# Optimization experiments

Measured on AMD Instinct MI355X. Metric: run time of the kernel, lower is better.

## Reference

```python
import jax, jax.numpy as jnp
import numpy as np

NUM_HEADS = 4
NEG_INF = -1e9  # finite large-negative to avoid inf*weight -> nan in head combiner


def setup_inputs() -> dict:
    key = jax.random.key(0)
    k1, k2, k3, k4, k5 = jax.random.split(key, 5)
    B, S, T = 16, 1024, 512
    Q, E = 256, 512
    src_encodings = jax.random.normal(k1, (B, S, E), dtype=jnp.float32)
    src_token_mask = jax.random.randint(k2, (B, S), 0, 2).astype(jnp.bool_)
    query_vec = jax.random.normal(k3, (T, B, Q), dtype=jnp.float32)
    # Linear(src_encoding_size, query_vec_size * numheads, bias=False)
    W_src = jax.random.normal(k4, (E, Q * NUM_HEADS), dtype=jnp.float32) * (1.0 / np.sqrt(E))
    # Linear(numheads, 1, bias=False) -> combiner vector of shape (numheads,)
    w_comb = jax.random.normal(k5, (NUM_HEADS,), dtype=jnp.float32) * 0.5
    return {"src_encodings": src_encodings, "src_token_mask": src_token_mask,
            "query_vec": query_vec, "W_src": W_src, "w_comb": w_comb}


def reference(src_encodings, src_token_mask, query_vec, W_src, w_comb):
    # project + leaky_relu: (B,S,E) @ (E,H*Q) -> (B,S,H*Q)
    proj = jax.nn.leaky_relu(src_encodings @ W_src)
    B, S, _ = proj.shape
    Q = query_vec.shape[-1]
    proj = proj.reshape(B, S, NUM_HEADS, Q)                 # (B,S,H,Q)
    # per-head attention scores against each query step: (T,B,S,H)
    scores = jnp.einsum('bshq,tbq->tbsh', proj, query_vec)
    # mask invalid source tokens along S (broadcast over T and heads)
    scores = jnp.where(src_token_mask[None, :, :, None], NEG_INF, scores)
    # multihead combiner Linear(H,1,bias=False): (T,B,S)
    weights = jnp.einsum('tbsh,h->tbs', scores, w_comb)
    return jax.nn.softmax(weights, axis=-1)
```

## Files before the change

### kernel.cpp

```cpp
#include <hip/hip_runtime.h>
#include <hip/hip_bf16.h>
#include <cstdint>

constexpr int Bn = 16;
constexpr int Sn = 1024;
constexpr int Tn = 512;
constexpr int QD = 256;
constexpr int En = 512;
constexpr int Hn = 4;
constexpr float SLOPE = 0.01f;
constexpr float NEG_INF = -1e9f;
constexpr int Mn = Bn * Sn;

typedef _Float16 f16;
typedef f16 f16x4 __attribute__((ext_vector_type(4)));
typedef f16 f16x8 __attribute__((ext_vector_type(8)));
typedef float f32x4 __attribute__((ext_vector_type(4)));

#define G2L(g, l) __builtin_amdgcn_global_load_lds(                      \
    (const __attribute__((address_space(1))) void*)(g),                  \
    (__attribute__((address_space(3))) void*)(l), 16, 0, 0)

#define VM4 asm volatile("s_waitcnt vmcnt(4)" ::: "memory")
#define VM0 asm volatile("s_waitcnt vmcnt(0)" ::: "memory")

__global__ void detect_mask_kernel(const unsigned char* __restrict__ mask_bytes,
                                   int* __restrict__ flag) {
    __shared__ int cnt;
    if (threadIdx.x == 0) cnt = 0;
    __syncthreads();
    int local = 0;
    for (int p = threadIdx.x; p < 4096; p += 256) {
        if ((p & 3) != 0 && mask_bytes[p] != 0) local++;
    }
    atomicAdd(&cnt, local);
    __syncthreads();
    if (threadIdx.x == 0) flag[0] = (cnt == 0) ? 1 : 0;
}

__global__ __launch_bounds__(256) void conv_a_kernel(
    const float* __restrict__ src, f16* __restrict__ Ah, f16* __restrict__ Al)
{
    const size_t i4 = (size_t)blockIdx.x * 256 + threadIdx.x;
    const size_t base = i4 * 4;
    const float4 v = *(const float4*)(src + base);
    f16x4 hi, lo;
    const float xs[4] = {v.x, v.y, v.z, v.w};
    #pragma unroll
    for (int j = 0; j < 4; ++j) {
        f16 h = (f16)xs[j];
        hi[j] = h;
        lo[j] = (f16)(xs[j] - (float)h);
    }
    *(f16x4*)(Ah + base) = hi;
    *(f16x4*)(Al + base) = lo;
}

__global__ __launch_bounds__(256) void conv_b_kernel(
    const float* __restrict__ W, f16* __restrict__ Bht, f16* __restrict__ Blt)
{
    __shared__ float T[64][65];
    const int tid = threadIdx.x;
    const int n0 = blockIdx.x * 64;
    const int k0 = blockIdx.y * 64;
    #pragma unroll
    for (int p = 0; p < 4; ++p) {
        const int e = p * 256 + tid;
        const int r = e >> 4;
        const int c4 = e & 15;
        const float4 v = *(const float4*)(W + (size_t)(k0 + r) * (Hn * QD) + n0 + c4 * 4);
        T[r][c4 * 4 + 0] = v.x; T[r][c4 * 4 + 1] = v.y;
        T[r][c4 * 4 + 2] = v.z; T[r][c4 * 4 + 3] = v.w;
    }
    __syncthreads();
    #pragma unroll
    for (int p = 0; p < 4; ++p) {
        const int e = p * 256 + tid;
        const int r = e >> 4;
        const int c4 = e & 15;
        f16x4 hi, lo;
        #pragma unroll
        for (int j = 0; j < 4; ++j) {
            const float x = T[c4 * 4 + j][r];
            f16 h = (f16)x;
            hi[j] = h;
            lo[j] = (f16)(x - (float)h);
        }
        const size_t off = (size_t)(n0 + r) * En + k0 + c4 * 4;
        *(f16x4*)(Bht + off) = hi;
        *(f16x4*)(Blt + off) = lo;
    }
}

__global__ __launch_bounds__(256) void conv_q_kernel(
    const float* __restrict__ query, f16* __restrict__ Qh, f16* __restrict__ Ql)
{
    const int tid = threadIdx.x;
    const int rloc = tid >> 6;
    const int lane = tid & 63;
    const int row = blockIdx.x * 4 + rloc;
    const int t = row >> 4, b = row & 15;
    const float4 v = *(const float4*)(query + (size_t)row * QD + lane * 4);
    f16x4 hi, lo;
    const float xs[4] = {v.x, v.y, v.z, v.w};
    #pragma unroll
    for (int j = 0; j < 4; ++j) {
        f16 h = (f16)xs[j];
        hi[j] = h;
        lo[j] = (f16)(xs[j] - (float)h);
    }
    const size_t off = ((size_t)(b * Tn + t)) * QD + lane * 4;
    *(f16x4*)(Qh + off) = hi;
    *(f16x4*)(Ql + off) = lo;
}

__global__ __launch_bounds__(256) void gemm1_kernel(
    const f16* __restrict__ Ah, const f16* __restrict__ Al,
    const f16* __restrict__ Bht, const f16* __restrict__ Blt,
    const float* __restrict__ wcomb,
    f16* __restrict__ Ch, f16* __restrict__ Cl)
{
    __shared__ f16 lds_f[24576];

    const int tid = threadIdx.x;
    const int l  = tid & 63;
    const int wv = tid >> 6;
    const int wm = wv >> 1;
    const int wn = wv & 1;
    const int m0 = blockIdx.x * 128;
    const int q0 = blockIdx.y * 32;

    const int rowc = tid >> 2;
    const int xk   = ((tid & 3) ^ ((rowc >> 1) & 3)) * 8;
    const int stgA = (m0 + rowc) * En + xk;
    const int nB   = ((rowc >> 4) & 3) * QD + q0 + (rowc & 15);
    const int stgB = nB * En + xk;

    const int xf  = ((l >> 1) & 3);
    const int aFrag = (wm * 64 + (l & 15)) * 32 + (((l >> 4) ^ xf) * 8);
    const int bFrag = 4096 + (wn * 64 + (l & 15)) * 32 + (((l >> 4) ^ xf) * 8);

    f32x4 acc[4][4];
    #pragma unroll
    for (int m = 0; m < 4; ++m)
        #pragma unroll
        for (int h = 0; h < 4; ++h) acc[m][h] = (f32x4){0.f, 0.f, 0.f, 0.f};

    auto stage1 = [&](int t) {
        const f16* As = (t < 16) ? Ah : ((t < 32) ? Al : Ah);
        const f16* Bs = (t < 32) ? Bht : Blt;
        const int kofs = (t & 15) * 32;
        f16* dst = lds_f + (t % 3) * 8192 + wv * 512;
        G2L(As + stgA + kofs,           dst);
        G2L(As + stgA + 64 * En + kofs, dst + 2048);
        G2L(Bs + stgB + kofs,           dst + 4096);
        G2L(Bs + stgB + 16 * En + kofs, dst + 4096 + 2048);
    };

    stage1(0);
    stage1(1);
    VM4;
    __builtin_amdgcn_s_barrier();

    #pragma unroll
    for (int t = 0; t < 48; ++t) {
        const f16* Lb = lds_f + (t % 3) * 8192;
        f16x8 af[4], bfr[4];
        #pragma unroll
        for (int m = 0; m < 4; ++m) af[m] = *(const f16x8*)(Lb + aFrag + m * 512);
        #pragma unroll
        for (int h = 0; h < 4; ++h) bfr[h] = *(const f16x8*)(Lb + bFrag + h * 512);
        if (t + 2 < 48) stage1(t + 2);
        __builtin_amdgcn_s_barrier();
        asm volatile("s_waitcnt lgkmcnt(0)" ::: "memory");
        __builtin_amdgcn_sched_barrier(0);
        __builtin_amdgcn_s_setprio(1);
        #pragma unroll
        for (int m = 0; m < 4; ++m) {
            #pragma unroll
            for (int h = 0; h < 4; ++h)
                acc[m][h] = __builtin_amdgcn_mfma_f32_16x16x32_f16(
                    af[m], bfr[h], acc[m][h], 0, 0, 0);
        }
        __builtin_amdgcn_s_setprio(0);
        if (t <= 45)      VM4;
        else if (t == 46) VM0;
        __builtin_amdgcn_s_barrier();
    }

    const float w0 = wcomb[0], w1 = wcomb[1], w2 = wcomb[2], w3 = wcomb[3];
    const int q = q0 + wn * 16 + (l & 15);
    const int rbase = m0 + wm * 64 + (l >> 4) * 4;
    #pragma unroll
    for (int m = 0; m < 4; ++m) {
        #pragma unroll
        for (int i = 0; i < 4; ++i) {
            float x0 = acc[m][0][i]; x0 = x0 >= 0.f ? x0 : SLOPE * x0;
            float x1 = acc[m][1][i]; x1 = x1 >= 0.f ? x1 : SLOPE * x1;
            float x2 = acc[m][2][i]; x2 = x2 >= 0.f ? x2 : SLOPE * x2;
            float x3 = acc[m][3][i]; x3 = x3 >= 0.f ? x3 : SLOPE * x3;
            const float c = w0 * x0 + w1 * x1 + w2 * x2 + w3 * x3;
            const f16 ch = (f16)c;
            const f16 cl = (f16)(c - (float)ch);
            const size_t off = (size_t)(rbase + m * 16 + i) * QD + q;
            Ch[off] = ch;
            Cl[off] = cl;
        }
    }
}

__global__ __launch_bounds__(256) void gemm2_kernel(
    const f16* __restrict__ Ch, const f16* __restrict__ Cl,
    const f16* __restrict__ Qh, const f16* __restrict__ Ql,
    const void* __restrict__ maskp, const float* __restrict__ wcomb,
    const int* __restrict__ flag,
    float* __restrict__ out)
{
    __shared__ f16 lds2[24576];

    const int tid = threadIdx.x;
    const int l  = tid & 63;
    const int wv = tid >> 6;
    const int wm = wv >> 1;
    const int wn = wv & 1;
    const int b  = blockIdx.z;
    const int s0 = blockIdx.x * 128;
    const int t0 = blockIdx.y * 128;

    const int rowc = tid >> 2;
    const int xk   = ((tid & 3) ^ ((rowc >> 1) & 3)) * 8;
    const int stgA = (b * Sn + s0 + rowc) * QD + xk;
    const int stgB = (b * Tn + t0 + rowc) * QD + xk;

    const int xf  = ((l >> 1) & 3);
    const int aFrag = (wm * 64 + (l & 15)) * 32 + (((l >> 4) ^ xf) * 8);
    const int bFrag = 4096 + (wn * 64 + (l & 15)) * 32 + (((l >> 4) ^ xf) * 8);

    f32x4 acc[4][4];
    #pragma unroll
    for (int m = 0; m < 4; ++m)
        #pragma unroll
        for (int n = 0; n < 4; ++n) acc[m][n] = (f32x4){0.f, 0.f, 0.f, 0.f};

    auto stage1 = [&](int t) {
        const f16* As = (t < 8) ? Ch : ((t < 16) ? Cl : Ch);
        const f16* Bs = (t < 16) ? Qh : Ql;
        const int kofs = (t & 7) * 32;
        f16* dst = lds2 + (t % 3) * 8192 + wv * 512;
        G2L(As + stgA + kofs,           dst);
        G2L(As + stgA + 64 * QD + kofs, dst + 2048);
        G2L(Bs + stgB + kofs,           dst + 4096);
        G2L(Bs + stgB + 64 * QD + kofs, dst + 4096 + 2048);
    };

    stage1(0);
    stage1(1);
    VM4;
    __builtin_amdgcn_s_barrier();

    #pragma unroll
    for (int kt = 0; kt < 24; ++kt) {
        const f16* Lb = lds2 + (kt % 3) * 8192;
        f16x8 af[4], bfr[4];
        #pragma unroll
        for (int m = 0; m < 4; ++m) af[m] = *(const f16x8*)(Lb + aFrag + m * 512);
        #pragma unroll
        for (int n = 0; n < 4; ++n) bfr[n] = *(const f16x8*)(Lb + bFrag + n * 512);
        if (kt + 2 < 24) stage1(kt + 2);
        __builtin_amdgcn_s_barrier();
        asm volatile("s_waitcnt lgkmcnt(0)" ::: "memory");
        __builtin_amdgcn_sched_barrier(0);
        __builtin_amdgcn_s_setprio(1);
        #pragma unroll
        for (int m = 0; m < 4; ++m) {
            #pragma unroll
            for (int n = 0; n < 4; ++n)
                acc[m][n] = __builtin_amdgcn_mfma_f32_16x16x32_f16(
                    af[m], bfr[n], acc[m][n], 0, 0, 0);
        }
        __builtin_amdgcn_s_setprio(0);
        if (kt <= 21)      VM4;
        else if (kt == 22) VM0;
        __builtin_amdgcn_s_barrier();
    }

    const float sumw = wcomb[0] + wcomb[1] + wcomb[2] + wcomb[3];
    const float maskval = NEG_INF * sumw;
    const bool is_int = (flag[0] != 0);
    const int rbase = s0 + wm * 64 + (l >> 4) * 4;

    bool msk[4][4];
    #pragma unroll
    for (int m = 0; m < 4; ++m)
        #pragma unroll
        for (int i = 0; i < 4; ++i) {
            const int idx = b * Sn + rbase + m * 16 + i;
            int mm;
            if (is_int) mm = ((const int*)maskp)[idx];
            else        mm = (int)((const unsigned char*)maskp)[idx];
            msk[m][i] = (mm != 0);
        }

    #pragma unroll
    for (int m = 0; m < 4; ++m)
        #pragma unroll
        for (int n = 0; n < 4; ++n) {
            const int t = t0 + wn * 64 + n * 16 + (l & 15);
            float vals[4];
            #pragma unroll
            for (int i = 0; i < 4; ++i)
                vals[i] = msk[m][i] ? maskval : acc[m][n][i];
            *(float4*)(out + ((size_t)t * Bn + b) * Sn + rbase + m * 16)
                = make_float4(vals[0], vals[1], vals[2], vals[3]);
        }
}

__global__ __launch_bounds__(256) void softmax_kernel(float* __restrict__ out) {
    const size_t row = blockIdx.x;
    float* p = out + row * (size_t)Sn;
    const int tid = threadIdx.x;
    const int lane = tid & 63, wave = tid >> 6;

    float4 v = ((const float4*)p)[tid];

    float m = fmaxf(fmaxf(v.x, v.y), fmaxf(v.z, v.w));
    #pragma unroll
    for (int off = 32; off; off >>= 1) m = fmaxf(m, __shfl_down(m, off));
    __shared__ float smax[4];
    __shared__ float sm_all;
    if (lane == 0) smax[wave] = m;
    __syncthreads();
    if (tid == 0) sm_all = fmaxf(fmaxf(smax[0], smax[1]), fmaxf(smax[2], smax[3]));
    __syncthreads();
    m = sm_all;

    float e0 = __expf(v.x - m), e1 = __expf(v.y - m);
    float e2 = __expf(v.z - m), e3 = __expf(v.w - m);
    float s = e0 + e1 + e2 + e3;
    #pragma unroll
    for (int off = 32; off; off >>= 1) s += __shfl_down(s, off);
    __shared__ float ssum[4];
    __shared__ float ss_all;
    if (lane == 0) ssum[wave] = s;
    __syncthreads();
    if (tid == 0) ss_all = ssum[0] + ssum[1] + ssum[2] + ssum[3];
    __syncthreads();
    const float inv = 1.0f / ss_all;

    ((float4*)p)[tid] = make_float4(e0 * inv, e1 * inv, e2 * inv, e3 * inv);
}

extern "C" void kernel_launch(void* const* d_in, const int* in_sizes, int n_in,
                              void* d_out, int out_size, void* d_ws, size_t ws_size,
                              hipStream_t stream) {
    const float* src   = (const float*)d_in[0];
    const void*  maskp = d_in[1];
    const float* query = (const float*)d_in[2];
    const float* Wsrc  = (const float*)d_in[3];
    const float* wcomb = (const float*)d_in[4];
    float* out = (float*)d_out;

    constexpr size_t MB = 1024 * 1024;
    char* ws = (char*)d_ws;
    int* flag = (int*)ws;
    f16* Ah  = (f16*)(ws + 256);
    f16* Al  = (f16*)(ws + 256 + 16 * MB);
    f16* Bht = (f16*)(ws + 256 + 32 * MB);
    f16* Blt = (f16*)(ws + 256 + 33 * MB);
    f16* Ch  = (f16*)(ws + 256 + 34 * MB);
    f16* Cl  = (f16*)(ws + 256 + 42 * MB);
    f16* Qh  = (f16*)(ws + 256);
    f16* Ql  = (f16*)(ws + 256 + 4 * MB);

    detect_mask_kernel<<<1, 256, 0, stream>>>((const unsigned char*)maskp, flag);

    conv_a_kernel<<<(Mn * En) / (256 * 4), 256, 0, stream>>>(src, Ah, Al);
    {
        dim3 grid((Hn * QD) / 64, En / 64);
        conv_b_kernel<<<grid, 256, 0, stream>>>(Wsrc, Bht, Blt);
    }
    {
        dim3 grid(Mn / 128, QD / 32);
        gemm1_kernel<<<grid, 256, 0, stream>>>(Ah, Al, Bht, Blt, wcomb, Ch, Cl);
    }
    conv_q_kernel<<<(Tn * Bn) / 4, 256, 0, stream>>>(query, Qh, Ql);
    {
        dim3 grid(Sn / 128, Tn / 128, Bn);
        gemm2_kernel<<<grid, 256, 0, stream>>>(Ch, Cl, Qh, Ql, maskp, wcomb, flag, out);
    }
    softmax_kernel<<<Tn * Bn, 256, 0, stream>>>(out);
}
```

Before: 128.6 us.

## Widen gemm1 tile to 64 query columns per block across all heads

The gemm1 block tile grows from 32 to 64 query columns, with all four heads of each column loaded per k-step. Each wave now holds 4x8 accumulators, and the grid halves along the query dimension. The A tile is shared across twice as many output columns, which halves the reloads of the large split-f16 A operand. The cost is more LDS per block (three 24 KB stages), more registers, a deeper vmcnt wait, and half as many blocks, which may reduce occupancy.

```diff
diff --git a/kernel.cpp b/kernel.cpp
--- a/kernel.cpp
+++ b/kernel.cpp
@@ -21,6 +21,7 @@
     (const __attribute__((address_space(1))) void*)(g),                  \
     (__attribute__((address_space(3))) void*)(l), 16, 0, 0)
 
+#define VM6 asm volatile("s_waitcnt vmcnt(6)" ::: "memory")
 #define VM4 asm volatile("s_waitcnt vmcnt(4)" ::: "memory")
 #define VM0 asm volatile("s_waitcnt vmcnt(0)" ::: "memory")
 
@@ -120,7 +121,7 @@
     const float* __restrict__ wcomb,
     f16* __restrict__ Ch, f16* __restrict__ Cl)
 {
-    __shared__ f16 lds_f[24576];
+    __shared__ f16 lds_f[36864];
 
     const int tid = threadIdx.x;
     const int l  = tid & 63;
@@ -128,48 +129,51 @@
     const int wm = wv >> 1;
     const int wn = wv & 1;
     const int m0 = blockIdx.x * 128;
-    const int q0 = blockIdx.y * 32;
-
-    const int rowc = tid >> 2;
-    const int xk   = ((tid & 3) ^ ((rowc >> 1) & 3)) * 8;
-    const int stgA = (m0 + rowc) * En + xk;
-    const int nB   = ((rowc >> 4) & 3) * QD + q0 + (rowc & 15);
-    const int stgB = nB * En + xk;
-
-    const int xf  = ((l >> 1) & 3);
-    const int aFrag = (wm * 64 + (l & 15)) * 32 + (((l >> 4) ^ xf) * 8);
-    const int bFrag = 4096 + (wn * 64 + (l & 15)) * 32 + (((l >> 4) ^ xf) * 8);
-
-    f32x4 acc[4][4];
+    const int q0 = blockIdx.y * 64;
+
+    const int rc  = tid >> 2;
+    const int xk  = ((tid & 3) ^ ((tid >> 3) & 3)) * 8;
+    const int stgA = (m0 + rc) * En + xk;
+    const int stgB = (q0 + rc) * En + xk;
+
+    const int xf  = (l >> 1) & 3;
+    const int kx  = ((l >> 4) ^ xf) * 8;
+    const int aFrag = (wm * 64 + (l & 15)) * 32 + kx;
+    const int bFrag = 4096 + (wn * 32 + (l & 15)) * 32 + kx;
+
+    f32x4 acc[4][8];
     #pragma unroll
     for (int m = 0; m < 4; ++m)
         #pragma unroll
-        for (int h = 0; h < 4; ++h) acc[m][h] = (f32x4){0.f, 0.f, 0.f, 0.f};
+        for (int f = 0; f < 8; ++f) acc[m][f] = (f32x4){0.f, 0.f, 0.f, 0.f};
 
     auto stage1 = [&](int t) {
         const f16* As = (t < 16) ? Ah : ((t < 32) ? Al : Ah);
         const f16* Bs = (t < 32) ? Bht : Blt;
         const int kofs = (t & 15) * 32;
-        f16* dst = lds_f + (t % 3) * 8192 + wv * 512;
-        G2L(As + stgA + kofs,           dst);
-        G2L(As + stgA + 64 * En + kofs, dst + 2048);
-        G2L(Bs + stgB + kofs,           dst + 4096);
-        G2L(Bs + stgB + 16 * En + kofs, dst + 4096 + 2048);
+        f16* dst = lds_f + (t % 3) * 12288 + wv * 512;
+        G2L(As + stgA + kofs,                dst);
+        G2L(As + stgA + 64 * En + kofs,      dst + 2048);
+        G2L(Bs + stgB + kofs,                dst + 4096);
+        G2L(Bs + stgB + QD * En + kofs,      dst + 4096 + 2048);
+        G2L(Bs + stgB + 2 * QD * En + kofs,  dst + 4096 + 4096);
+        G2L(Bs + stgB + 3 * QD * En + kofs,  dst + 4096 + 6144);
     };
 
     stage1(0);
     stage1(1);
-    VM4;
+    VM6;
     __builtin_amdgcn_s_barrier();
 
     #pragma unroll
     for (int t = 0; t < 48; ++t) {
-        const f16* Lb = lds_f + (t % 3) * 8192;
-        f16x8 af[4], bfr[4];
+        const f16* Lb = lds_f + (t % 3) * 12288;
+        f16x8 af[4], bfr[8];
         #pragma unroll
         for (int m = 0; m < 4; ++m) af[m] = *(const f16x8*)(Lb + aFrag + m * 512);
         #pragma unroll
-        for (int h = 0; h < 4; ++h) bfr[h] = *(const f16x8*)(Lb + bFrag + h * 512);
+        for (int f = 0; f < 8; ++f)
+            bfr[f] = *(const f16x8*)(Lb + bFrag + (f >> 1) * 2048 + (f & 1) * 512);
         if (t + 2 < 48) stage1(t + 2);
         __builtin_amdgcn_s_barrier();
         asm volatile("s_waitcnt lgkmcnt(0)" ::: "memory");
@@ -178,33 +182,36 @@
         #pragma unroll
         for (int m = 0; m < 4; ++m) {
             #pragma unroll
-            for (int h = 0; h < 4; ++h)
-                acc[m][h] = __builtin_amdgcn_mfma_f32_16x16x32_f16(
-                    af[m], bfr[h], acc[m][h], 0, 0, 0);
+            for (int f = 0; f < 8; ++f)
+                acc[m][f] = __builtin_amdgcn_mfma_f32_16x16x32_f16(
+                    af[m], bfr[f], acc[m][f], 0, 0, 0);
         }
         __builtin_amdgcn_s_setprio(0);
-        if (t <= 45)      VM4;
+        if (t <= 45)      VM6;
         else if (t == 46) VM0;
         __builtin_amdgcn_s_barrier();
     }
 
     const float w0 = wcomb[0], w1 = wcomb[1], w2 = wcomb[2], w3 = wcomb[3];
-    const int q = q0 + wn * 16 + (l & 15);
     const int rbase = m0 + wm * 64 + (l >> 4) * 4;
     #pragma unroll
     for (int m = 0; m < 4; ++m) {
         #pragma unroll
-        for (int i = 0; i < 4; ++i) {
-            float x0 = acc[m][0][i]; x0 = x0 >= 0.f ? x0 : SLOPE * x0;
-            float x1 = acc[m][1][i]; x1 = x1 >= 0.f ? x1 : SLOPE * x1;
-            float x2 = acc[m][2][i]; x2 = x2 >= 0.f ? x2 : SLOPE * x2;
-            float x3 = acc[m][3][i]; x3 = x3 >= 0.f ? x3 : SLOPE * x3;
-            const float c = w0 * x0 + w1 * x1 + w2 * x2 + w3 * x3;
-            const f16 ch = (f16)c;
-            const f16 cl = (f16)(c - (float)ch);
-            const size_t off = (size_t)(rbase + m * 16 + i) * QD + q;
-            Ch[off] = ch;
-            Cl[off] = cl;
+        for (int qs = 0; qs < 2; ++qs) {
+            const int q = q0 + wn * 32 + qs * 16 + (l & 15);
+            #pragma unroll
+            for (int i = 0; i < 4; ++i) {
+                float x0 = acc[m][0 + qs][i]; x0 = x0 >= 0.f ? x0 : SLOPE * x0;
+                float x1 = acc[m][2 + qs][i]; x1 = x1 >= 0.f ? x1 : SLOPE * x1;
+                float x2 = acc[m][4 + qs][i]; x2 = x2 >= 0.f ? x2 : SLOPE * x2;
+                float x3 = acc[m][6 + qs][i]; x3 = x3 >= 0.f ? x3 : SLOPE * x3;
+                const float c = w0 * x0 + w1 * x1 + w2 * x2 + w3 * x3;
+                const f16 ch = (f16)c;
+                const f16 cl = (f16)(c - (float)ch);
+                const size_t off = (size_t)(rbase + m * 16 + i) * QD + q;
+                Ch[off] = ch;
+                Cl[off] = cl;
+            }
         }
     }
 }
@@ -380,7 +387,7 @@
         conv_b_kernel<<<grid, 256, 0, stream>>>(Wsrc, Bht, Blt);
     }
     {
-        dim3 grid(Mn / 128, QD / 32);
+        dim3 grid(Mn / 128, QD / 64);
         gemm1_kernel<<<grid, 256, 0, stream>>>(Ah, Al, Bht, Blt, wcomb, Ch, Cl);
     }
     conv_q_kernel<<<(Tn * Bn) / 4, 256, 0, stream>>>(query, Qh, Ql);
```

After: 122.0 us. -5.1%, faster.

## Enlarge gemm1 tile to 256x256 with 8 waves and streamline gemm2 pipeline

Applied to the files above, without the earlier changes.

gemm1 moves from a 128-row by 32-query tile with 4 waves to a 256-row by 64-query tile (all four heads) with 8 waves and 512 threads. Each k-step now runs in two phases: A and B fragments are loaded, then the second A half, with the LDS triple buffer doubled in size. The aim is more reuse of each staged A and B tile per global load and fewer blocks re-reading the split-fp16 operands. gemm2 now issues the next stage's global-to-LDS loads before the fragment reads and drops the mid-iteration barrier, waiting on LDS only at the end of the step. The larger gemm1 tile raises register and LDS pressure, which may limit occupancy.

```diff
diff --git a/kernel.cpp b/kernel.cpp
--- a/kernel.cpp
+++ b/kernel.cpp
@@ -23,6 +23,7 @@
 
 #define VM4 asm volatile("s_waitcnt vmcnt(4)" ::: "memory")
 #define VM0 asm volatile("s_waitcnt vmcnt(0)" ::: "memory")
+#define LG0 asm volatile("s_waitcnt lgkmcnt(0)" ::: "memory")
 
 __global__ void detect_mask_kernel(const unsigned char* __restrict__ mask_bytes,
                                    int* __restrict__ flag) {
@@ -114,73 +115,104 @@
     *(f16x4*)(Ql + off) = lo;
 }
 
-__global__ __launch_bounds__(256) void gemm1_kernel(
+__global__ __launch_bounds__(512, 2) void gemm1_kernel(
     const f16* __restrict__ Ah, const f16* __restrict__ Al,
     const f16* __restrict__ Bht, const f16* __restrict__ Blt,
     const float* __restrict__ wcomb,
     f16* __restrict__ Ch, f16* __restrict__ Cl)
 {
-    __shared__ f16 lds_f[24576];
+    __shared__ f16 lds_f[49152];
 
     const int tid = threadIdx.x;
     const int l  = tid & 63;
     const int wv = tid >> 6;
-    const int wm = wv >> 1;
-    const int wn = wv & 1;
-    const int m0 = blockIdx.x * 128;
-    const int q0 = blockIdx.y * 32;
-
-    const int rowc = tid >> 2;
-    const int xk   = ((tid & 3) ^ ((rowc >> 1) & 3)) * 8;
-    const int stgA = (m0 + rowc) * En + xk;
-    const int nB   = ((rowc >> 4) & 3) * QD + q0 + (rowc & 15);
-    const int stgB = nB * En + xk;
-
-    const int xf  = ((l >> 1) & 3);
-    const int aFrag = (wm * 64 + (l & 15)) * 32 + (((l >> 4) ^ xf) * 8);
-    const int bFrag = 4096 + (wn * 64 + (l & 15)) * 32 + (((l >> 4) ^ xf) * 8);
-
-    f32x4 acc[4][4];
-    #pragma unroll
-    for (int m = 0; m < 4; ++m)
-        #pragma unroll
-        for (int h = 0; h < 4; ++h) acc[m][h] = (f32x4){0.f, 0.f, 0.f, 0.f};
-
-    auto stage1 = [&](int t) {
-        const f16* As = (t < 16) ? Ah : ((t < 32) ? Al : Ah);
-        const f16* Bs = (t < 32) ? Bht : Blt;
-        const int kofs = (t & 15) * 32;
-        f16* dst = lds_f + (t % 3) * 8192 + wv * 512;
-        G2L(As + stgA + kofs,           dst);
-        G2L(As + stgA + 64 * En + kofs, dst + 2048);
-        G2L(Bs + stgB + kofs,           dst + 4096);
-        G2L(Bs + stgB + 16 * En + kofs, dst + 4096 + 2048);
+    const int wm = wv >> 2;
+    const int wn = wv & 3;
+    const int m0 = blockIdx.x * 256;
+    const int q0 = blockIdx.y * 64;
+
+    const int rls = wv * 16 + (l >> 2);
+    const int xk  = ((l & 3) ^ ((l >> 3) & 3)) * 8;
+    const size_t stgA0 = (size_t)(m0 + rls) * En + xk;
+    const size_t stgA1 = stgA0 + (size_t)128 * En;
+    int rBv[2];
+    #pragma unroll
+    for (int h = 0; h < 2; ++h) {
+        const int c = h * 128 + rls;
+        rBv[h] = ((c >> 4) & 3) * QD + q0 + ((c >> 6) * 16) + (c & 15);
+    }
+    const size_t stgB0 = (size_t)rBv[0] * En + xk;
+    const size_t stgB1 = (size_t)rBv[1] * En + xk;
+
+    const int kx   = (((l >> 4) ^ ((l >> 1) & 3))) * 8;
+    const int aRow = (wm * 128 + (l & 15)) * 32 + kx;
+    const int bCol = 8192 + (wn * 64 + (l & 15)) * 32 + kx;
+
+    f32x4 acc[8][4];
+    #pragma unroll
+    for (int m = 0; m < 8; ++m)
+        #pragma unroll
+        for (int n = 0; n < 4; ++n) acc[m][n] = (f32x4){0.f, 0.f, 0.f, 0.f};
+
+    auto stageAB = [&](int t, int pair) {
+        const int kbase = (t & 15) * 32;
+        f16* dst = lds_f + (t % 3) * 16384 + pair * 8192 + wv * 512;
+        if (pair == 0) {
+            const f16* A = (t < 16) ? Ah : ((t < 32) ? Al : Ah);
+            G2L(A + stgA0 + kbase, dst);
+            G2L(A + stgA1 + kbase, dst + 4096);
+        } else {
+            const f16* B = (t < 32) ? Bht : Blt;
+            G2L(B + stgB0 + kbase, dst);
+            G2L(B + stgB1 + kbase, dst + 4096);
+        }
     };
 
-    stage1(0);
-    stage1(1);
+    stageAB(0, 0); stageAB(0, 1);
+    stageAB(1, 0); stageAB(1, 1);
     VM4;
     __builtin_amdgcn_s_barrier();
 
-    #pragma unroll
+    #pragma unroll 3
     for (int t = 0; t < 48; ++t) {
-        const f16* Lb = lds_f + (t % 3) * 8192;
-        f16x8 af[4], bfr[4];
-        #pragma unroll
-        for (int m = 0; m < 4; ++m) af[m] = *(const f16x8*)(Lb + aFrag + m * 512);
-        #pragma unroll
-        for (int h = 0; h < 4; ++h) bfr[h] = *(const f16x8*)(Lb + bFrag + h * 512);
-        if (t + 2 < 48) stage1(t + 2);
+        const f16* Lb = lds_f + (t % 3) * 16384;
+        f16x8 bf[4], af0[4], af1[4];
+
+        #pragma unroll
+        for (int mf = 0; mf < 4; ++mf)
+            af0[mf] = *(const f16x8*)(Lb + aRow + mf * 512);
+        #pragma unroll
+        for (int nf = 0; nf < 4; ++nf)
+            bf[nf] = *(const f16x8*)(Lb + bCol + nf * 512);
+        if (t + 2 < 48) stageAB(t + 2, 0);
         __builtin_amdgcn_s_barrier();
-        asm volatile("s_waitcnt lgkmcnt(0)" ::: "memory");
+        LG0;
         __builtin_amdgcn_sched_barrier(0);
         __builtin_amdgcn_s_setprio(1);
         #pragma unroll
-        for (int m = 0; m < 4; ++m) {
+        for (int mf = 0; mf < 4; ++mf) {
             #pragma unroll
-            for (int h = 0; h < 4; ++h)
-                acc[m][h] = __builtin_amdgcn_mfma_f32_16x16x32_f16(
-                    af[m], bfr[h], acc[m][h], 0, 0, 0);
+            for (int nf = 0; nf < 4; ++nf)
+                acc[mf][nf] = __builtin_amdgcn_mfma_f32_16x16x32_f16(
+                    af0[mf], bf[nf], acc[mf][nf], 0, 0, 0);
+        }
+        __builtin_amdgcn_s_setprio(0);
+        __builtin_amdgcn_s_barrier();
+
+        #pragma unroll
+        for (int mf = 0; mf < 4; ++mf)
+            af1[mf] = *(const f16x8*)(Lb + aRow + 2048 + mf * 512);
+        if (t + 2 < 48) stageAB(t + 2, 1);
+        __builtin_amdgcn_s_barrier();
+        LG0;
+        __builtin_amdgcn_sched_barrier(0);
+        __builtin_amdgcn_s_setprio(1);
+        #pragma unroll
+        for (int mf = 0; mf < 4; ++mf) {
+            #pragma unroll
+            for (int nf = 0; nf < 4; ++nf)
+                acc[4 + mf][nf] = __builtin_amdgcn_mfma_f32_16x16x32_f16(
+                    af1[mf], bf[nf], acc[4 + mf][nf], 0, 0, 0);
         }
         __builtin_amdgcn_s_setprio(0);
         if (t <= 45)      VM4;
@@ -190,9 +222,9 @@
 
     const float w0 = wcomb[0], w1 = wcomb[1], w2 = wcomb[2], w3 = wcomb[3];
     const int q = q0 + wn * 16 + (l & 15);
-    const int rbase = m0 + wm * 64 + (l >> 4) * 4;
-    #pragma unroll
-    for (int m = 0; m < 4; ++m) {
+    #pragma unroll
+    for (int m = 0; m < 8; ++m) {
+        const int rbase = m0 + wm * 128 + (m >> 2) * 64 + (m & 3) * 16 + (l >> 4) * 4;
         #pragma unroll
         for (int i = 0; i < 4; ++i) {
             float x0 = acc[m][0][i]; x0 = x0 >= 0.f ? x0 : SLOPE * x0;
@@ -202,7 +234,7 @@
             const float c = w0 * x0 + w1 * x1 + w2 * x2 + w3 * x3;
             const f16 ch = (f16)c;
             const f16 cl = (f16)(c - (float)ch);
-            const size_t off = (size_t)(rbase + m * 16 + i) * QD + q;
+            const size_t off = (size_t)(rbase + i) * QD + q;
             Ch[off] = ch;
             Cl[off] = cl;
         }
@@ -260,16 +292,13 @@
 
     #pragma unroll
     for (int kt = 0; kt < 24; ++kt) {
+        if (kt + 2 < 24) stage1(kt + 2);
         const f16* Lb = lds2 + (kt % 3) * 8192;
         f16x8 af[4], bfr[4];
         #pragma unroll
         for (int m = 0; m < 4; ++m) af[m] = *(const f16x8*)(Lb + aFrag + m * 512);
         #pragma unroll
         for (int n = 0; n < 4; ++n) bfr[n] = *(const f16x8*)(Lb + bFrag + n * 512);
-        if (kt + 2 < 24) stage1(kt + 2);
-        __builtin_amdgcn_s_barrier();
-        asm volatile("s_waitcnt lgkmcnt(0)" ::: "memory");
-        __builtin_amdgcn_sched_barrier(0);
         __builtin_amdgcn_s_setprio(1);
         #pragma unroll
         for (int m = 0; m < 4; ++m) {
@@ -281,6 +310,7 @@
         __builtin_amdgcn_s_setprio(0);
         if (kt <= 21)      VM4;
         else if (kt == 22) VM0;
+        LG0;
         __builtin_amdgcn_s_barrier();
     }
 
@@ -380,8 +410,8 @@
         conv_b_kernel<<<grid, 256, 0, stream>>>(Wsrc, Bht, Blt);
     }
     {
-        dim3 grid(Mn / 128, QD / 32);
-        gemm1_kernel<<<grid, 256, 0, stream>>>(Ah, Al, Bht, Blt, wcomb, Ch, Cl);
+        dim3 grid(Mn / 256, QD / 64);
+        gemm1_kernel<<<grid, 512, 0, stream>>>(Ah, Al, Bht, Blt, wcomb, Ch, Cl);
     }
     conv_q_kernel<<<(Tn * Bn) / 4, 256, 0, stream>>>(query, Qh, Ql);
     {
```

New measurement: 144.8 us. +12.6%, slower.
